# Kernel tuning notes

Measured on AMD Instinct MI355X. Metric: run time of the kernel, lower is better.

The kernel has to match this reference:

```python
import jax, jax.numpy as jnp
import numpy as np

N = 4096
BATCH = 1024


def setup_inputs() -> dict:
    key = jax.random.key(0)
    k1, k2, k3 = jax.random.split(key, 3)
    stdv = 1.0 / np.sqrt(N)
    return {
        "input": jax.random.normal(k1, (BATCH, N), dtype=jnp.float32),
        "weight": jax.random.uniform(k2, (N,), dtype=jnp.float32, minval=-stdv, maxval=stdv),
        "bias": jax.random.uniform(k3, (N,), dtype=jnp.float32, minval=-stdv, maxval=stdv),
    }


def reference(input, weight, bias):
    # Krylov(shift, w) has columns K[:, k] = shift^k(w), i.e. K[i, k] = w[(i - k) mod n].
    # F.linear(x, K.T, b) = x @ (K.T).T + b = x @ K + b.
    n = weight.shape[0]
    i = jnp.arange(n)
    idx = (i[:, None] - i[None, :]) % n        # [n, n] circulant index pattern
    K = weight[idx]                            # [n, n] circulant matrix
    return input @ K + bias
```

## Files before the change

kernel.cpp:

```cpp
#include <hip/hip_runtime.h>

typedef short s8v __attribute__((ext_vector_type(8)));
typedef float f4v __attribute__((ext_vector_type(4)));
typedef float f16v __attribute__((ext_vector_type(16)));

#define ND 4096
#define NMASK 4095

__device__ __forceinline__ unsigned short f2bf(float f) {
  __bf16 h = (__bf16)f;
  return __builtin_bit_cast(unsigned short, h);
}

__device__ __forceinline__ void gload_lds16(const void* g, void* l) {
  __builtin_amdgcn_global_load_lds(
      (const __attribute__((address_space(1))) unsigned int*)g,
      (__attribute__((address_space(3))) unsigned int*)l, 16, 0, 0);
}

__global__ __launch_bounds__(256)
void prep(const float* __restrict__ X, const float* __restrict__ W,
          unsigned short* __restrict__ Xpk, unsigned int* __restrict__ wlg) {
  const int b = blockIdx.x;
  const int tid = threadIdx.x;
  if (b < 1024) {
    const int r0 = (b & 15) << 6;
    const int k0 = (b >> 4) << 6;
    const int r = tid >> 2;
    const int kseg = tid & 3;
    const int row = r0 + r;
    const int k = k0 + (kseg << 4);
    const float* src = X + row * ND + k;
    const f4v g0 = *(const f4v*)(src + 0);
    const f4v g1 = *(const f4v*)(src + 4);
    const f4v g2 = *(const f4v*)(src + 8);
    const f4v g3 = *(const f4v*)(src + 12);
    s8v u0, u1;
    #pragma unroll
    for (int j = 0; j < 4; ++j) {
      u0[j] = (short)f2bf(g0[j]); u0[4 + j] = (short)f2bf(g1[j]);
      u1[j] = (short)f2bf(g2[j]); u1[4 + j] = (short)f2bf(g3[j]);
    }
    const int o0 = k >> 3;
    *(s8v*)(Xpk + ((o0 * 1024 + row) << 3))       = u0;
    *(s8v*)(Xpk + (((o0 + 1) * 1024 + row) << 3)) = u1;
  } else {
    const int m = (b - 1024) * 256 + tid;
    const int e0 = m << 1, e1 = e0 + 1;
    const int i0 = ((e0 >> 3) + (e0 & 7)) & NMASK;
    const int i1 = ((e1 >> 3) + (e1 & 7)) & NMASK;
    wlg[m] = (unsigned int)f2bf(W[i0]) | ((unsigned int)f2bf(W[i1]) << 16);
  }
}

__global__ __launch_bounds__(256, 2)
void circ_mm(const unsigned short* __restrict__ Xpk,
             const unsigned short* __restrict__ wlg,
             const float* __restrict__ bias, float* __restrict__ C) {
  extern __shared__ unsigned short smem[];
  unsigned char* __restrict__ sb = (unsigned char*)smem;

  const int tid = threadIdx.x;
  const int bid = blockIdx.x;
  const int x = bid & 7;
  const int i = bid >> 3;
  const int m0 = (x + ((i >> 5) << 3)) << 6;
  const int n0 = (i & 31) << 7;

  const int lane = tid & 63;
  const int wv = tid >> 6;
  const int kb = wv;

  #pragma unroll
  for (int it = 0; it < 16; ++it) {
    const int b = it * 4096 + (wv << 10);
    gload_lds16((const unsigned char*)wlg + b + lane * 16, sb + b);
  }

  const int lc = lane & 31;
  const int lh = lane >> 5;
  const int lh8 = lh << 3;

  const unsigned short* gXa =
      Xpk + ((((kb << 1) + lh) << 10) + m0 + lc) * 8;

  int s0 = ((kb << 4) + lh8 - (n0 + 0 * 32 + lc)) & NMASK;
  int s1 = ((kb << 4) + lh8 - (n0 + 1 * 32 + lc)) & NMASK;
  int s2 = ((kb << 4) + lh8 - (n0 + 2 * 32 + lc)) & NMASK;
  int s3 = ((kb << 4) + lh8 - (n0 + 3 * 32 + lc)) & NMASK;

  f16v acc[2][4];
  #pragma unroll
  for (int mf = 0; mf < 2; ++mf)
    #pragma unroll
    for (int nf = 0; nf < 4; ++nf)
      #pragma unroll
      for (int e = 0; e < 16; ++e) acc[mf][nf][e] = 0.f;

  s8v Ab[3][2];
  s8v Bb[2][4];

  Ab[0][0] = *(const s8v*)(gXa + 0);
  Ab[0][1] = *(const s8v*)(gXa + 256);
  Ab[1][0] = *(const s8v*)(gXa + 65536);
  Ab[1][1] = *(const s8v*)(gXa + 65536 + 256);
  __syncthreads();
  Bb[0][0] = *(const s8v*)(sb + (s0 << 4));
  Bb[0][1] = *(const s8v*)(sb + (s1 << 4));
  Bb[0][2] = *(const s8v*)(sb + (s2 << 4));
  Bb[0][3] = *(const s8v*)(sb + (s3 << 4));

  #pragma unroll
  for (int t = 0; t < 64; ++t) {
    if (t + 2 < 64) {
      const unsigned short* gp = gXa + (t + 2) * 65536;
      Ab[(t + 2) % 3][0] = *(const s8v*)(gp + 0);
      Ab[(t + 2) % 3][1] = *(const s8v*)(gp + 256);
    }
    if (t + 1 < 64) {
      s0 = (s0 + 64) & NMASK;
      s1 = (s1 + 64) & NMASK;
      s2 = (s2 + 64) & NMASK;
      s3 = (s3 + 64) & NMASK;
      Bb[(t + 1) & 1][0] = *(const s8v*)(sb + (s0 << 4));
      Bb[(t + 1) & 1][1] = *(const s8v*)(sb + (s1 << 4));
      Bb[(t + 1) & 1][2] = *(const s8v*)(sb + (s2 << 4));
      Bb[(t + 1) & 1][3] = *(const s8v*)(sb + (s3 << 4));
    }

    const s8v a0 = Ab[t % 3][0];
    const s8v a1 = Ab[t % 3][1];
    __builtin_amdgcn_s_setprio(1);
    acc[0][0] = __builtin_amdgcn_mfma_f32_32x32x16_bf16(a0, Bb[t & 1][0], acc[0][0], 0, 0, 0);
    acc[1][0] = __builtin_amdgcn_mfma_f32_32x32x16_bf16(a1, Bb[t & 1][0], acc[1][0], 0, 0, 0);
    acc[0][1] = __builtin_amdgcn_mfma_f32_32x32x16_bf16(a0, Bb[t & 1][1], acc[0][1], 0, 0, 0);
    acc[1][1] = __builtin_amdgcn_mfma_f32_32x32x16_bf16(a1, Bb[t & 1][1], acc[1][1], 0, 0, 0);
    acc[0][2] = __builtin_amdgcn_mfma_f32_32x32x16_bf16(a0, Bb[t & 1][2], acc[0][2], 0, 0, 0);
    acc[1][2] = __builtin_amdgcn_mfma_f32_32x32x16_bf16(a1, Bb[t & 1][2], acc[1][2], 0, 0, 0);
    acc[0][3] = __builtin_amdgcn_mfma_f32_32x32x16_bf16(a0, Bb[t & 1][3], acc[0][3], 0, 0, 0);
    acc[1][3] = __builtin_amdgcn_mfma_f32_32x32x16_bf16(a1, Bb[t & 1][3], acc[1][3], 0, 0, 0);
    __builtin_amdgcn_s_setprio(0);
  }

  __syncthreads();
  float* red = (float*)smem;
  float* rb;

  if (kb >= 2) {
    rb = red + (kb - 2) * 8192;
    #pragma unroll
    for (int mf = 0; mf < 2; ++mf)
      #pragma unroll
      for (int nf = 0; nf < 4; ++nf)
        #pragma unroll
        for (int q = 0; q < 4; ++q) {
          const int j = (mf * 4 + nf) * 4 + q;
          f4v v;
          #pragma unroll
          for (int e = 0; e < 4; ++e) v[e] = acc[mf][nf][q * 4 + e];
          *(f4v*)(&rb[(j * 64 + lane) * 4]) = v;
        }
  }
  __syncthreads();
  if (kb < 2) {
    rb = red + kb * 8192;
    #pragma unroll
    for (int mf = 0; mf < 2; ++mf)
      #pragma unroll
      for (int nf = 0; nf < 4; ++nf)
        #pragma unroll
        for (int q = 0; q < 4; ++q) {
          const int j = (mf * 4 + nf) * 4 + q;
          const f4v v = *(const f4v*)(&rb[(j * 64 + lane) * 4]);
          #pragma unroll
          for (int e = 0; e < 4; ++e) acc[mf][nf][q * 4 + e] += v[e];
        }
  }
  __syncthreads();
  if (kb == 1) {
    rb = red;
    #pragma unroll
    for (int mf = 0; mf < 2; ++mf)
      #pragma unroll
      for (int nf = 0; nf < 4; ++nf)
        #pragma unroll
        for (int q = 0; q < 4; ++q) {
          const int j = (mf * 4 + nf) * 4 + q;
          f4v v;
          #pragma unroll
          for (int e = 0; e < 4; ++e) v[e] = acc[mf][nf][q * 4 + e];
          *(f4v*)(&rb[(j * 64 + lane) * 4]) = v;
        }
  }
  __syncthreads();
  if (kb == 0) {
    rb = red;
    #pragma unroll
    for (int mf = 0; mf < 2; ++mf)
      #pragma unroll
      for (int nf = 0; nf < 4; ++nf)
        #pragma unroll
        for (int q = 0; q < 4; ++q) {
          const int j = (mf * 4 + nf) * 4 + q;
          const f4v v = *(const f4v*)(&rb[(j * 64 + lane) * 4]);
          #pragma unroll
          for (int e = 0; e < 4; ++e) acc[mf][nf][q * 4 + e] += v[e];
        }
    const int lh4 = lh << 2;
    #pragma unroll
    for (int nf = 0; nf < 4; ++nf) {
      const int col = n0 + nf * 32 + lc;
      const float bv = bias[col];
      #pragma unroll
      for (int mf = 0; mf < 2; ++mf)
        #pragma unroll
        for (int g = 0; g < 4; ++g) {
          const int row = m0 + mf * 32 + g * 8 + lh4;
          #pragma unroll
          for (int e = 0; e < 4; ++e)
            C[(row + e) * ND + col] = acc[mf][nf][g * 4 + e] + bv;
        }
    }
  }
}

extern "C" void kernel_launch(void* const* d_in, const int* in_sizes, int n_in,
                              void* d_out, int out_size, void* d_ws, size_t ws_size,
                              hipStream_t stream) {
  (void)hipFuncSetAttribute((const void*)circ_mm,
                            hipFuncAttributeMaxDynamicSharedMemorySize, 65536);
  const float* X    = (const float*)d_in[0];
  const float* W    = (const float*)d_in[1];
  const float* bias = (const float*)d_in[2];
  unsigned short* wlg = (unsigned short*)d_ws;
  unsigned short* Xpk = (unsigned short*)d_ws + 32768;

  prep<<<dim3(1088), dim3(256), 0, stream>>>(X, W, Xpk, (unsigned int*)wlg);
  circ_mm<<<dim3(512), dim3(256), 65536, stream>>>(Xpk, wlg, bias, (float*)d_out);
}
```

Measured before the change: 40.31 us.

## Distribute split-K epilogue reduction and stores across all four waves

```diff
diff --git a/kernel.cpp b/kernel.cpp
--- a/kernel.cpp
+++ b/kernel.cpp
@@ -142,86 +142,103 @@
     __builtin_amdgcn_s_setprio(0);
   }
 
+  #define ACC_EL(j, e) (acc[(j) >> 4][((j) >> 2) & 3][((j) & 3) * 4 + (e)])
+
   __syncthreads();
   float* red = (float*)smem;
-  float* rb;
-
-  if (kb >= 2) {
-    rb = red + (kb - 2) * 8192;
-    #pragma unroll
-    for (int mf = 0; mf < 2; ++mf)
-      #pragma unroll
-      for (int nf = 0; nf < 4; ++nf)
+
+  if (kb == 2 || kb == 3) {
+    float* rb = red + (kb - 2) * 8192;
+    #pragma unroll
+    for (int j = 0; j < 32; ++j) {
+      f4v v;
+      #pragma unroll
+      for (int e = 0; e < 4; ++e) v[e] = ACC_EL(j, e);
+      *(f4v*)(&rb[(j * 64 + lane) * 4]) = v;
+    }
+  }
+  __syncthreads();
+  if (kb == 0) {
+    float* rb = red;
+    #pragma unroll
+    for (int j = 0; j < 32; ++j) {
+      const f4v v = *(const f4v*)(&rb[(j * 64 + lane) * 4]);
+      #pragma unroll
+      for (int e = 0; e < 4; ++e) ACC_EL(j, e) += v[e];
+    }
+    #pragma unroll
+    for (int j = 8; j < 32; ++j) {
+      f4v v;
+      #pragma unroll
+      for (int e = 0; e < 4; ++e) v[e] = ACC_EL(j, e);
+      *(f4v*)(&rb[(j * 64 + lane) * 4]) = v;
+    }
+  }
+  if (kb == 1) {
+    float* rb = red + 8192;
+    #pragma unroll
+    for (int j = 0; j < 32; ++j) {
+      const f4v v = *(const f4v*)(&rb[(j * 64 + lane) * 4]);
+      #pragma unroll
+      for (int e = 0; e < 4; ++e) ACC_EL(j, e) += v[e];
+    }
+    #pragma unroll
+    for (int j = 0; j < 8; ++j) {
+      f4v v;
+      #pragma unroll
+      for (int e = 0; e < 4; ++e) v[e] = ACC_EL(j, e);
+      *(f4v*)(&rb[(j * 64 + lane) * 4]) = v;
+    }
+    #pragma unroll
+    for (int j = 16; j < 32; ++j) {
+      f4v v;
+      #pragma unroll
+      for (int e = 0; e < 4; ++e) v[e] = ACC_EL(j, e);
+      *(f4v*)(&rb[(j * 64 + lane) * 4]) = v;
+    }
+  }
+  __syncthreads();
+
+  {
+    const int lh4 = lh << 2;
+    const int nfb = (kb & 1) * 2;
+    float bv[2];
+    bv[0] = bias[n0 + (nfb + 0) * 32 + lc];
+    bv[1] = bias[n0 + (nfb + 1) * 32 + lc];
+
+    #pragma unroll
+    for (int jj = 0; jj < 8; ++jj) {
+      f4v v;
+      if (kb == 0) {
+        const int j = jj;
+        const f4v w = *(const f4v*)(&red[8192 + (j * 64 + lane) * 4]);
         #pragma unroll
-        for (int q = 0; q < 4; ++q) {
-          const int j = (mf * 4 + nf) * 4 + q;
-          f4v v;
-          #pragma unroll
-          for (int e = 0; e < 4; ++e) v[e] = acc[mf][nf][q * 4 + e];
-          *(f4v*)(&rb[(j * 64 + lane) * 4]) = v;
-        }
-  }
-  __syncthreads();
-  if (kb < 2) {
-    rb = red + kb * 8192;
-    #pragma unroll
-    for (int mf = 0; mf < 2; ++mf)
-      #pragma unroll
-      for (int nf = 0; nf < 4; ++nf)
+        for (int e = 0; e < 4; ++e) v[e] = ACC_EL(j, e) + w[e];
+      } else if (kb == 1) {
+        const int j = 8 + jj;
+        const f4v w = *(const f4v*)(&red[(j * 64 + lane) * 4]);
         #pragma unroll
-        for (int q = 0; q < 4; ++q) {
-          const int j = (mf * 4 + nf) * 4 + q;
-          const f4v v = *(const f4v*)(&rb[(j * 64 + lane) * 4]);
-          #pragma unroll
-          for (int e = 0; e < 4; ++e) acc[mf][nf][q * 4 + e] += v[e];
-        }
-  }
-  __syncthreads();
-  if (kb == 1) {
-    rb = red;
-    #pragma unroll
-    for (int mf = 0; mf < 2; ++mf)
-      #pragma unroll
-      for (int nf = 0; nf < 4; ++nf)
+        for (int e = 0; e < 4; ++e) v[e] = ACC_EL(j, e) + w[e];
+      } else {
+        const int j = kb * 8 + jj;
+        const f4v w0 = *(const f4v*)(&red[(j * 64 + lane) * 4]);
+        const f4v w1 = *(const f4v*)(&red[8192 + (j * 64 + lane) * 4]);
         #pragma unroll
-        for (int q = 0; q < 4; ++q) {
-          const int j = (mf * 4 + nf) * 4 + q;
-          f4v v;
-          #pragma unroll
-          for (int e = 0; e < 4; ++e) v[e] = acc[mf][nf][q * 4 + e];
-          *(f4v*)(&rb[(j * 64 + lane) * 4]) = v;
-        }
-  }
-  __syncthreads();
-  if (kb == 0) {
-    rb = red;
-    #pragma unroll
-    for (int mf = 0; mf < 2; ++mf)
-      #pragma unroll
-      for (int nf = 0; nf < 4; ++nf)
-        #pragma unroll
-        for (int q = 0; q < 4; ++q) {
-          const int j = (mf * 4 + nf) * 4 + q;
-          const f4v v = *(const f4v*)(&rb[(j * 64 + lane) * 4]);
-          #pragma unroll
-          for (int e = 0; e < 4; ++e) acc[mf][nf][q * 4 + e] += v[e];
-        }
-    const int lh4 = lh << 2;
-    #pragma unroll
-    for (int nf = 0; nf < 4; ++nf) {
+        for (int e = 0; e < 4; ++e) v[e] = w0[e] + w1[e];
+      }
+      const int j = kb * 8 + jj;
+      const int mf = j >> 4;
+      const int nf = (j >> 2) & 3;
+      const int q  = j & 3;
       const int col = n0 + nf * 32 + lc;
-      const float bv = bias[col];
-      #pragma unroll
-      for (int mf = 0; mf < 2; ++mf)
-        #pragma unroll
-        for (int g = 0; g < 4; ++g) {
-          const int row = m0 + mf * 32 + g * 8 + lh4;
-          #pragma unroll
-          for (int e = 0; e < 4; ++e)
-            C[(row + e) * ND + col] = acc[mf][nf][g * 4 + e] + bv;
-        }
-    }
-  }
+      const int row = m0 + mf * 32 + q * 8 + lh4;
+      const float b = bv[nf - nfb];
+      #pragma unroll
+      for (int e = 0; e < 4; ++e)
+        C[(row + e) * ND + col] = v[e] + b;
+    }
+  }
+  #undef ACC_EL
 }
 
 extern "C" void kernel_launch(void* const* d_in, const int* in_sizes, int n_in,
```

Result: faster. 39.32 us (-2.4%).
